# Optimization experiments

Measured on AMD Instinct MI355X. Metric: run time of the kernel, lower is better.

The kernel has to match this reference:

```python
import jax, jax.numpy as jnp
import numpy as np

B, T, D, U = 32, 2048, 512, 512


def setup_inputs() -> dict:
    key = jax.random.key(0)
    ks = jax.random.split(key, 6)
    value = jax.random.normal(ks[0], (B, T, D), dtype=jnp.float32)
    query = jax.random.normal(ks[1], (B, D), dtype=jnp.float32)
    mask = jax.random.randint(ks[2], (B, T), 0, 2, dtype=jnp.int32)
    # Glorot-ish scaled dense weights (no bias, matching Dense(use_bias=False))
    W1 = jax.random.normal(ks[3], (D, U), dtype=jnp.float32) * (1.0 / np.sqrt(D))
    W2 = jax.random.normal(ks[4], (D, U), dtype=jnp.float32) * (1.0 / np.sqrt(D))
    V = jax.random.normal(ks[5], (U,), dtype=jnp.float32) * (1.0 / np.sqrt(U))
    return {"value": value, "query": query, "mask": mask, "W1": W1, "W2": W2, "V": V}


def reference(value, query, mask, W1, W2, V):
    # Additive (Bahdanau) attention scores: u[b,t] = V . tanh(value[b,t] @ W1 + query[b] @ W2)
    w1_key = jnp.einsum('btd,du->btu', value, W1)          # [B, T, U]
    w2_query = jnp.einsum('bd,du->bu', query, W2)          # [B, U]
    u = jnp.einsum('btu,u->bt', jnp.tanh(w1_key + w2_query[:, None, :]), V)  # [B, T]
    # Masking: add -1e20 where mask == 0 (same as keras reference)
    u = u + (1.0 - mask.astype(u.dtype)) * jnp.asarray(-1e20, dtype=u.dtype)
    a = jax.nn.softmax(u, axis=1)                          # [B, T]
    # Pointer extraction: gather value row at argmax of attention weights
    idx = jnp.argmax(a, axis=1)                            # [B]
    context = jnp.take_along_axis(value, idx[:, None, None], axis=1)[:, 0, :]  # [B, D]
    return (context, a)
```

## Files before the change

kernel.cpp:

```cpp
#include <hip/hip_runtime.h>
#include <hip/hip_bf16.h>
#include <hip/hip_fp16.h>
#include <stdint.h>

#define B_ 32
#define T_ 2048
#define D_ 512
#define U_ 512
#define M_ (B_ * T_)

#define BM 64
#define BK 32
#define SAW 40
#define MAXC 4

typedef _Float16 half8  __attribute__((ext_vector_type(8)));
typedef _Float16 half4_t __attribute__((ext_vector_type(4)));
typedef float   floatx4 __attribute__((ext_vector_type(4)));

__device__ __forceinline__ float tanh_fast(float x) {
    float ax = fabsf(x);
    float e  = __expf(2.0f * ax);
    float t  = 1.0f - 2.0f / (e + 1.0f);
    return copysignf(t, x);
}

__device__ __forceinline__ void gld_lds16(const void* gsrc, void* lds_dst) {
    typedef __attribute__((address_space(1))) const char gch;
    typedef __attribute__((address_space(3))) char lch;
    __builtin_amdgcn_global_load_lds((const gch*)(uintptr_t)gsrc,
                                     (lch*)(uint32_t)(uintptr_t)lds_dst,
                                     16, 0, 0);
}

__global__ __launch_bounds__(256)
void k_prep(const float* __restrict__ W1, const float* __restrict__ query,
            const float* __restrict__ W2, _Float16* __restrict__ W1T,
            float* __restrict__ w2q) {
    const int bid = blockIdx.x;
    const int tid = threadIdx.x;
    if (bid < 64) {
        __shared__ float tile[64][65];
        const int bx = bid & 7;
        const int by = bid >> 3;
        const int k0 = bx * 64, n0 = by * 64;
        const int tx = tid & 63;
        const int ty = tid >> 6;
#pragma unroll
        for (int i = 0; i < 16; ++i) {
            int r = ty * 16 + i;
            tile[r][tx] = W1[(size_t)(k0 + r) * U_ + n0 + tx];
        }
        __syncthreads();
#pragma unroll
        for (int i = 0; i < 16; ++i) {
            int r = ty * 16 + i;
            W1T[(size_t)(n0 + r) * D_ + k0 + tx] = (_Float16)tile[tx][r];
        }
    } else {
        __shared__ float sq[D_];
        __shared__ float part[128];
        const int id = bid - 64;
        const int b  = id >> 2;
        const int nq = id & 3;
        sq[tid]       = query[b * D_ + tid];
        sq[tid + 256] = query[b * D_ + tid + 256];
        __syncthreads();
        const int n  = nq * 128 + (tid & 127);
        const int dh = tid >> 7;
        float acc = 0.f;
        const int d0 = dh * 256;
#pragma unroll 16
        for (int d = d0; d < d0 + 256; ++d)
            acc = fmaf(sq[d], W2[(size_t)d * U_ + n], acc);
        if (dh == 1) part[tid & 127] = acc;
        __syncthreads();
        if (dh == 0) w2q[b * U_ + n] = acc + part[tid];
    }
}

__global__ __launch_bounds__(512, 4)
void k_gemm_u(const float* __restrict__ value,
              const _Float16* __restrict__ W1T,
              const float* __restrict__ w2q,
              const float* __restrict__ Vv,
              float* __restrict__ u_out) {
    __shared__ __align__(16) _Float16 sA[2][BM * SAW];
    __shared__ __align__(16) _Float16 sB[2][U_ * BK];
    __shared__ float sRed[8][BM];

    const int tid  = threadIdx.x;
    const int wave = tid >> 6;
    const int lane = tid & 63;
    const int l15  = lane & 15;
    const int lg   = lane >> 4;
    const int m0   = blockIdx.x * BM;
    const int b    = m0 >> 11;

    const int bnl  = l15;
    const int bhi8 = lg * 8;

    const int ar = tid >> 3;
    const int ac = (tid & 7) * 4;
    const float* aptr = value + (size_t)(m0 + ar) * D_ + ac;

    floatx4 rA[2];

    rA[0] = *(const floatx4*)(aptr);
    rA[1] = *(const floatx4*)(aptr + BK);
#pragma unroll
    for (int jj = 0; jj < 4; ++jj) {
        const int inst = wave * 4 + jj;
        const int n = inst * 16 + bnl;
        gld_lds16(W1T + (size_t)n * D_ + bhi8, (void*)(&sB[0][inst * 512]));
    }
    {
        half4_t h;
        h[0] = (_Float16)rA[0][0]; h[1] = (_Float16)rA[0][1];
        h[2] = (_Float16)rA[0][2]; h[3] = (_Float16)rA[0][3];
        *(half4_t*)(&sA[0][ar * SAW + ac]) = h;
    }

    floatx4 acc[4][4];
    const floatx4 zero4 = {0.f, 0.f, 0.f, 0.f};
#pragma unroll
    for (int i = 0; i < 4; ++i)
#pragma unroll
        for (int j = 0; j < 4; ++j) acc[i][j] = zero4;

    __syncthreads();

    for (int kk = 0; kk < 16; ++kk) {
        const int cur = kk & 1;
        if (kk < 15) {
            const int k0n = (kk + 1) * BK;
#pragma unroll
            for (int jj = 0; jj < 4; ++jj) {
                const int inst = wave * 4 + jj;
                const int n = inst * 16 + bnl;
                gld_lds16(W1T + (size_t)n * D_ + k0n + bhi8,
                          (void*)(&sB[cur ^ 1][inst * 512]));
            }
        }
        if (kk < 14) rA[cur] = *(const floatx4*)(aptr + (kk + 2) * BK);

        half8 af[4], bf[4];
#pragma unroll
        for (int mi = 0; mi < 4; ++mi)
            af[mi] = *(const half8*)(&sA[cur][(mi * 16 + l15) * SAW + lg * 8]);
#pragma unroll
        for (int ni = 0; ni < 4; ++ni) {
            const int inst = wave * 4 + ni;
            bf[ni] = *(const half8*)(&sB[cur][inst * 512 + (lg * 16 + l15) * 8]);
        }
#pragma unroll
        for (int ni = 0; ni < 4; ++ni)
#pragma unroll
            for (int mi = 0; mi < 4; ++mi)
                acc[mi][ni] = __builtin_amdgcn_mfma_f32_16x16x32_f16(
                    af[mi], bf[ni], acc[mi][ni], 0, 0, 0);

        if (kk < 15) {
            const floatx4 v4 = rA[cur ^ 1];
            half4_t h;
            h[0] = (_Float16)v4[0]; h[1] = (_Float16)v4[1];
            h[2] = (_Float16)v4[2]; h[3] = (_Float16)v4[3];
            *(half4_t*)(&sA[cur ^ 1][ar * SAW + ac]) = h;
        }
        __syncthreads();
    }

    float ps[4][4];
#pragma unroll
    for (int mi = 0; mi < 4; ++mi)
#pragma unroll
        for (int j = 0; j < 4; ++j) ps[mi][j] = 0.f;

#pragma unroll
    for (int ni = 0; ni < 4; ++ni) {
        const int n = wave * 64 + ni * 16 + l15;
        const float w2 = w2q[b * U_ + n];
        const float vv = Vv[n];
#pragma unroll
        for (int mi = 0; mi < 4; ++mi)
#pragma unroll
            for (int j = 0; j < 4; ++j)
                ps[mi][j] += vv * tanh_fast(acc[mi][ni][j] + w2);
    }
#pragma unroll
    for (int off = 1; off < 16; off <<= 1)
#pragma unroll
        for (int mi = 0; mi < 4; ++mi)
#pragma unroll
            for (int j = 0; j < 4; ++j)
                ps[mi][j] += __shfl_xor(ps[mi][j], off, 64);

    if (l15 == 0) {
#pragma unroll
        for (int mi = 0; mi < 4; ++mi)
#pragma unroll
            for (int j = 0; j < 4; ++j)
                sRed[wave][mi * 16 + lg * 4 + j] = ps[mi][j];
    }
    __syncthreads();
    if (tid < BM) {
        float s = 0.f;
#pragma unroll
        for (int w = 0; w < 8; ++w) s += sRed[w][tid];
        u_out[m0 + tid] = s;
    }
}

__global__ __launch_bounds__(256)
void k_post(const float* __restrict__ u, const int* __restrict__ mask,
            const float* __restrict__ value, const float* __restrict__ W1,
            const float* __restrict__ w2q, const float* __restrict__ Vv,
            float* __restrict__ a_out, float* __restrict__ ctx_out) {
    __shared__ float sx[T_];
    __shared__ float rv[4];
    __shared__ int   ri[4];
    __shared__ float s_scalar;
    __shared__ int   s_cand[MAXC];
    __shared__ float s_score[MAXC];
    __shared__ __align__(16) float vrows[MAXC][D_];
    __shared__ int   s_t;

    const int b = blockIdx.x;
    const int tid = threadIdx.x;
    const int wave = tid >> 6, lane = tid & 63;

#pragma unroll
    for (int i = 0; i < 8; ++i) {
        const int t = tid * 8 + i;
        float x = u[b * T_ + t];
        if (mask[b * T_ + t] == 0) x = -1e20f;
        sx[t] = x;
    }
    __syncthreads();

    for (int r = 0; r < MAXC; ++r) {
        float v = -INFINITY; int vi = 0;
#pragma unroll
        for (int i = 0; i < 8; ++i) {
            const int t = tid * 8 + i;
            const float x = sx[t];
            if (x > v) { v = x; vi = t; }
        }
        for (int off = 32; off > 0; off >>= 1) {
            const float ov = __shfl_down(v, off, 64);
            const int   oi = __shfl_down(vi, off, 64);
            if (ov > v || (ov == v && oi < vi)) { v = ov; vi = oi; }
        }
        if (lane == 0) { rv[wave] = v; ri[wave] = vi; }
        __syncthreads();
        if (tid == 0) {
            float bv = rv[0]; int bi = ri[0];
            for (int w = 1; w < 4; ++w)
                if (rv[w] > bv || (rv[w] == bv && ri[w] < bi)) { bv = rv[w]; bi = ri[w]; }
            s_cand[r] = bi;
            if (r == 0) s_scalar = bv;
            sx[bi] = -INFINITY;
        }
        __syncthreads();
    }
    const float mx = s_scalar;

    float zloc = 0.f;
    float evals[8];
#pragma unroll
    for (int i = 0; i < 8; ++i) {
        const int t = tid * 8 + i;
        float x = u[b * T_ + t];
        if (mask[b * T_ + t] == 0) x = -1e20f;
        const float e = __expf(x - mx);
        evals[i] = e;
        zloc += e;
    }
    for (int off = 32; off > 0; off >>= 1) zloc += __shfl_down(zloc, off, 64);
    if (lane == 0) rv[wave] = zloc;
    __syncthreads();
    if (tid == 0) s_scalar = 1.0f / (rv[0] + rv[1] + rv[2] + rv[3]);
    __syncthreads();
    const float rz = s_scalar;
#pragma unroll
    for (int i = 0; i < 8; ++i) {
        const int t = tid * 8 + i;
        a_out[b * T_ + t] = evals[i] * rz;
    }

#pragma unroll
    for (int ci = 0; ci < MAXC; ++ci) {
        const int t = s_cand[ci];
        vrows[ci][tid]       = value[((size_t)b * T_ + t) * D_ + tid];
        vrows[ci][tid + 256] = value[((size_t)b * T_ + t) * D_ + tid + 256];
    }
    __syncthreads();

    float dots[2][MAXC];
#pragma unroll
    for (int j = 0; j < 2; ++j)
#pragma unroll
        for (int ci = 0; ci < MAXC; ++ci) dots[j][ci] = 0.f;

    for (int d4 = 0; d4 < D_; d4 += 4) {
        floatx4 vr[MAXC];
#pragma unroll
        for (int ci = 0; ci < MAXC; ++ci)
            vr[ci] = *(const floatx4*)(&vrows[ci][d4]);
#pragma unroll
        for (int k = 0; k < 4; ++k) {
            const float w0 = W1[(size_t)(d4 + k) * U_ + tid];
            const float w1 = W1[(size_t)(d4 + k) * U_ + tid + 256];
#pragma unroll
            for (int ci = 0; ci < MAXC; ++ci) {
                dots[0][ci] = fmaf(vr[ci][k], w0, dots[0][ci]);
                dots[1][ci] = fmaf(vr[ci][k], w1, dots[1][ci]);
            }
        }
    }
    float sc[MAXC];
#pragma unroll
    for (int ci = 0; ci < MAXC; ++ci) {
        const float n0v = Vv[tid]       * tanhf(dots[0][ci] + w2q[b * U_ + tid]);
        const float n1v = Vv[tid + 256] * tanhf(dots[1][ci] + w2q[b * U_ + tid + 256]);
        sc[ci] = n0v + n1v;
    }
#pragma unroll
    for (int ci = 0; ci < MAXC; ++ci)
        for (int off = 32; off > 0; off >>= 1)
            sc[ci] += __shfl_down(sc[ci], off, 64);
    __syncthreads();
    if (lane == 0) {
#pragma unroll
        for (int ci = 0; ci < MAXC; ++ci)
            vrows[ci][wave] = sc[ci];
    }
    __syncthreads();
    if (tid == 0) {
#pragma unroll
        for (int ci = 0; ci < MAXC; ++ci) {
            const int t = s_cand[ci];
            float s = vrows[ci][0] + vrows[ci][1] + vrows[ci][2] + vrows[ci][3];
            if (mask[b * T_ + t] == 0) s = -1e20f;
            s_score[ci] = s;
        }
        float bv = s_score[0]; int bt = s_cand[0];
        for (int i = 1; i < MAXC; ++i) {
            if (s_score[i] > bv || (s_score[i] == bv && s_cand[i] < bt)) {
                bv = s_score[i]; bt = s_cand[i];
            }
        }
        s_t = bt;
    }
    __syncthreads();

    const int t = s_t;
    ctx_out[b * D_ + tid]       = value[((size_t)b * T_ + t) * D_ + tid];
    ctx_out[b * D_ + tid + 256] = value[((size_t)b * T_ + t) * D_ + tid + 256];
}

extern "C" void kernel_launch(void* const* d_in, const int* in_sizes, int n_in,
                              void* d_out, int out_size, void* d_ws, size_t ws_size,
                              hipStream_t stream) {
    const float* value = (const float*)d_in[0];
    const float* query = (const float*)d_in[1];
    const int*   mask  = (const int*)d_in[2];
    const float* W1    = (const float*)d_in[3];
    const float* W2    = (const float*)d_in[4];
    const float* Vv    = (const float*)d_in[5];

    char* ws = (char*)d_ws;
    _Float16* W1T  = (_Float16*)ws;
    float*    w2q  = (float*)(ws + 524288);
    float*    u_ws = (float*)(ws + 524288 + 65536);

    float* ctx_out = (float*)d_out;
    float* a_out   = (float*)d_out + B_ * D_;

    hipLaunchKernelGGL(k_prep,   dim3(192), dim3(256), 0, stream,
                       W1, query, W2, W1T, w2q);
    hipLaunchKernelGGL(k_gemm_u, dim3(M_ / BM), dim3(512), 0, stream,
                       value, W1T, w2q, Vv, u_ws);
    hipLaunchKernelGGL(k_post,   dim3(32), dim3(256), 0, stream,
                       u_ws, mask, value, W1, w2q, Vv, a_out, ctx_out);
}
```

Before: 306.0 us.

## Rewrite GEMM as per-wave register-resident A tile with 32x32 MFMA, no LDS

Each wave now keeps its 32 rows of value, converted to fp16, fully in registers (32 half8 fragments). It streams W1T directly from global/L2 into 32x32x16 MFMAs for all 512 units and fuses tanh and the V dot product per 32-column group. LDS staging, double buffering and block-level syncs are gone, and the cross-wave reduction becomes a 32-lane shuffle reduce. In exchange, W1T is no longer shared through LDS, so every wave re-reads the full matrix from cache. The large register footprint also limits occupancy, and B-fragment loads are not prefetched or overlapped.

```diff
diff --git a/kernel.cpp b/kernel.cpp
--- a/kernel.cpp
+++ b/kernel.cpp
@@ -1,5 +1,4 @@
 #include <hip/hip_runtime.h>
-#include <hip/hip_bf16.h>
 #include <hip/hip_fp16.h>
 #include <stdint.h>
 
@@ -8,29 +7,17 @@
 #define D_ 512
 #define U_ 512
 #define M_ (B_ * T_)
-
-#define BM 64
-#define BK 32
-#define SAW 40
 #define MAXC 4
 
-typedef _Float16 half8  __attribute__((ext_vector_type(8)));
-typedef _Float16 half4_t __attribute__((ext_vector_type(4)));
-typedef float   floatx4 __attribute__((ext_vector_type(4)));
+typedef _Float16 half8   __attribute__((ext_vector_type(8)));
+typedef float   floatx4  __attribute__((ext_vector_type(4)));
+typedef float   floatx16 __attribute__((ext_vector_type(16)));
 
 __device__ __forceinline__ float tanh_fast(float x) {
     float ax = fabsf(x);
     float e  = __expf(2.0f * ax);
     float t  = 1.0f - 2.0f / (e + 1.0f);
     return copysignf(t, x);
-}
-
-__device__ __forceinline__ void gld_lds16(const void* gsrc, void* lds_dst) {
-    typedef __attribute__((address_space(1))) const char gch;
-    typedef __attribute__((address_space(3))) char lch;
-    __builtin_amdgcn_global_load_lds((const gch*)(uintptr_t)gsrc,
-                                     (lch*)(uint32_t)(uintptr_t)lds_dst,
-                                     16, 0, 0);
 }
 
 __global__ __launch_bounds__(256)
@@ -79,135 +66,81 @@
     }
 }
 
-__global__ __launch_bounds__(512, 4)
+__global__ __launch_bounds__(256, 2)
 void k_gemm_u(const float* __restrict__ value,
               const _Float16* __restrict__ W1T,
               const float* __restrict__ w2q,
               const float* __restrict__ Vv,
               float* __restrict__ u_out) {
-    __shared__ __align__(16) _Float16 sA[2][BM * SAW];
-    __shared__ __align__(16) _Float16 sB[2][U_ * BK];
-    __shared__ float sRed[8][BM];
-
     const int tid  = threadIdx.x;
     const int wave = tid >> 6;
     const int lane = tid & 63;
-    const int l15  = lane & 15;
-    const int lg   = lane >> 4;
-    const int m0   = blockIdx.x * BM;
+    const int l31  = lane & 31;
+    const int hi   = lane >> 5;
+    const int gw   = blockIdx.x * 4 + wave;
+    const int m0   = gw * 32;
     const int b    = m0 >> 11;
 
-    const int bnl  = l15;
-    const int bhi8 = lg * 8;
-
-    const int ar = tid >> 3;
-    const int ac = (tid & 7) * 4;
-    const float* aptr = value + (size_t)(m0 + ar) * D_ + ac;
-
-    floatx4 rA[2];
-
-    rA[0] = *(const floatx4*)(aptr);
-    rA[1] = *(const floatx4*)(aptr + BK);
-#pragma unroll
-    for (int jj = 0; jj < 4; ++jj) {
-        const int inst = wave * 4 + jj;
-        const int n = inst * 16 + bnl;
-        gld_lds16(W1T + (size_t)n * D_ + bhi8, (void*)(&sB[0][inst * 512]));
-    }
-    {
-        half4_t h;
-        h[0] = (_Float16)rA[0][0]; h[1] = (_Float16)rA[0][1];
-        h[2] = (_Float16)rA[0][2]; h[3] = (_Float16)rA[0][3];
-        *(half4_t*)(&sA[0][ar * SAW + ac]) = h;
-    }
-
-    floatx4 acc[4][4];
-    const floatx4 zero4 = {0.f, 0.f, 0.f, 0.f};
-#pragma unroll
-    for (int i = 0; i < 4; ++i)
-#pragma unroll
-        for (int j = 0; j < 4; ++j) acc[i][j] = zero4;
-
-    __syncthreads();
-
-    for (int kk = 0; kk < 16; ++kk) {
-        const int cur = kk & 1;
-        if (kk < 15) {
-            const int k0n = (kk + 1) * BK;
-#pragma unroll
-            for (int jj = 0; jj < 4; ++jj) {
-                const int inst = wave * 4 + jj;
-                const int n = inst * 16 + bnl;
-                gld_lds16(W1T + (size_t)n * D_ + k0n + bhi8,
-                          (void*)(&sB[cur ^ 1][inst * 512]));
+    half8 af[32];
+    const float* arow = value + (size_t)(m0 + l31) * D_ + hi * 8;
+#pragma unroll
+    for (int sb = 0; sb < 4; ++sb) {
+        floatx4 t0[8], t1[8];
+#pragma unroll
+        for (int s8 = 0; s8 < 8; ++s8) {
+            const float* p = arow + (sb * 8 + s8) * 16;
+            t0[s8] = *(const floatx4*)p;
+            t1[s8] = *(const floatx4*)(p + 4);
+        }
+#pragma unroll
+        for (int s8 = 0; s8 < 8; ++s8) {
+            half8 h;
+#pragma unroll
+            for (int j = 0; j < 4; ++j) {
+                h[j]     = (_Float16)t0[s8][j];
+                h[4 + j] = (_Float16)t1[s8][j];
             }
-        }
-        if (kk < 14) rA[cur] = *(const floatx4*)(aptr + (kk + 2) * BK);
-
-        half8 af[4], bf[4];
-#pragma unroll
-        for (int mi = 0; mi < 4; ++mi)
-            af[mi] = *(const half8*)(&sA[cur][(mi * 16 + l15) * SAW + lg * 8]);
-#pragma unroll
-        for (int ni = 0; ni < 4; ++ni) {
-            const int inst = wave * 4 + ni;
-            bf[ni] = *(const half8*)(&sB[cur][inst * 512 + (lg * 16 + l15) * 8]);
-        }
-#pragma unroll
-        for (int ni = 0; ni < 4; ++ni)
-#pragma unroll
-            for (int mi = 0; mi < 4; ++mi)
-                acc[mi][ni] = __builtin_amdgcn_mfma_f32_16x16x32_f16(
-                    af[mi], bf[ni], acc[mi][ni], 0, 0, 0);
-
-        if (kk < 15) {
-            const floatx4 v4 = rA[cur ^ 1];
-            half4_t h;
-            h[0] = (_Float16)v4[0]; h[1] = (_Float16)v4[1];
-            h[2] = (_Float16)v4[2]; h[3] = (_Float16)v4[3];
-            *(half4_t*)(&sA[cur ^ 1][ar * SAW + ac]) = h;
-        }
-        __syncthreads();
-    }
-
-    float ps[4][4];
-#pragma unroll
-    for (int mi = 0; mi < 4; ++mi)
-#pragma unroll
-        for (int j = 0; j < 4; ++j) ps[mi][j] = 0.f;
-
-#pragma unroll
-    for (int ni = 0; ni < 4; ++ni) {
-        const int n = wave * 64 + ni * 16 + l15;
+            af[sb * 8 + s8] = h;
+        }
+    }
+
+    float u_acc[16];
+#pragma unroll
+    for (int r = 0; r < 16; ++r) u_acc[r] = 0.f;
+
+    for (int g = 0; g < 16; ++g) {
+        const int n = g * 32 + l31;
+        const _Float16* bp = W1T + (size_t)n * D_ + hi * 8;
+
+        floatx16 acc;
+#pragma unroll
+        for (int r = 0; r < 16; ++r) acc[r] = 0.f;
+
+#pragma unroll
+        for (int s = 0; s < 32; ++s) {
+            const half8 bf = *(const half8*)(bp + s * 16);
+            acc = __builtin_amdgcn_mfma_f32_32x32x16_f16(af[s], bf, acc, 0, 0, 0);
+        }
+
         const float w2 = w2q[b * U_ + n];
         const float vv = Vv[n];
 #pragma unroll
-        for (int mi = 0; mi < 4; ++mi)
-#pragma unroll
-            for (int j = 0; j < 4; ++j)
-                ps[mi][j] += vv * tanh_fast(acc[mi][ni][j] + w2);
-    }
-#pragma unroll
-    for (int off = 1; off < 16; off <<= 1)
-#pragma unroll
-        for (int mi = 0; mi < 4; ++mi)
-#pragma unroll
-            for (int j = 0; j < 4; ++j)
-                ps[mi][j] += __shfl_xor(ps[mi][j], off, 64);
-
-    if (l15 == 0) {
-#pragma unroll
-        for (int mi = 0; mi < 4; ++mi)
-#pragma unroll
-            for (int j = 0; j < 4; ++j)
-                sRed[wave][mi * 16 + lg * 4 + j] = ps[mi][j];
-    }
-    __syncthreads();
-    if (tid < BM) {
-        float s = 0.f;
-#pragma unroll
-        for (int w = 0; w < 8; ++w) s += sRed[w][tid];
-        u_out[m0 + tid] = s;
+        for (int r = 0; r < 16; ++r)
+            u_acc[r] += vv * tanh_fast(acc[r] + w2);
+    }
+
+#pragma unroll
+    for (int off = 1; off < 32; off <<= 1)
+#pragma unroll
+        for (int r = 0; r < 16; ++r)
+            u_acc[r] += __shfl_xor(u_acc[r], off, 64);
+
+    if (l31 == 0) {
+#pragma unroll
+        for (int r = 0; r < 16; ++r) {
+            const int row = (r & 3) + 8 * (r >> 2) + 4 * hi;
+            u_out[m0 + row] = u_acc[r];
+        }
     }
 }
 
@@ -379,7 +312,7 @@
 
     hipLaunchKernelGGL(k_prep,   dim3(192), dim3(256), 0, stream,
                        W1, query, W2, W1T, w2q);
-    hipLaunchKernelGGL(k_gemm_u, dim3(M_ / BM), dim3(512), 0, stream,
+    hipLaunchKernelGGL(k_gemm_u, dim3(512), dim3(256), 0, stream,
                        value, W1T, w2q, Vv, u_ws);
     hipLaunchKernelGGL(k_post,   dim3(32), dim3(256), 0, stream,
                        u_ws, mask, value, W1, w2q, Vv, a_out, ctx_out);
```

Result: slower. 361.6 us (+18.2%).

## Split GEMM N dimension across two blocks, drop double buffering, sum partial scores

Applied to the files above, without the earlier changes.

The fused GEMM+tanh+V-dot kernel now gives each 64-row tile to two blocks, each covering half of the U columns (256). The two blocks write separate partial score vectors, and the post kernel adds them. LDS double buffering and register prefetch are removed to cut LDS and register use so more blocks fit per CU (launch bounds 4→5), and the grid doubles to 2048 blocks. The cost is that each 64-row value tile is read and converted twice, and load latency is no longer overlapped within a block.

```diff
diff --git a/kernel.cpp b/kernel.cpp
--- a/kernel.cpp
+++ b/kernel.cpp
@@ -1,5 +1,4 @@
 #include <hip/hip_runtime.h>
-#include <hip/hip_bf16.h>
 #include <hip/hip_fp16.h>
 #include <stdint.h>
 
@@ -8,15 +7,14 @@
 #define D_ 512
 #define U_ 512
 #define M_ (B_ * T_)
-
-#define BM 64
+#define MAXC 4
+
 #define BK 32
 #define SAW 40
-#define MAXC 4
-
-typedef _Float16 half8  __attribute__((ext_vector_type(8)));
+
+typedef _Float16 half8   __attribute__((ext_vector_type(8)));
 typedef _Float16 half4_t __attribute__((ext_vector_type(4)));
-typedef float   floatx4 __attribute__((ext_vector_type(4)));
+typedef float   floatx4  __attribute__((ext_vector_type(4)));
 
 __device__ __forceinline__ float tanh_fast(float x) {
     float ax = fabsf(x);
@@ -79,22 +77,25 @@
     }
 }
 
-__global__ __launch_bounds__(512, 4)
+__global__ __launch_bounds__(512, 5)
 void k_gemm_u(const float* __restrict__ value,
               const _Float16* __restrict__ W1T,
               const float* __restrict__ w2q,
               const float* __restrict__ Vv,
-              float* __restrict__ u_out) {
-    __shared__ __align__(16) _Float16 sA[2][BM * SAW];
-    __shared__ __align__(16) _Float16 sB[2][U_ * BK];
-    __shared__ float sRed[8][BM];
+              float* __restrict__ u_part) {
+    __shared__ __align__(16) _Float16 sA[64 * SAW];
+    __shared__ __align__(16) _Float16 sB[256 * BK];
+    __shared__ float sRed[8][64];
 
     const int tid  = threadIdx.x;
     const int wave = tid >> 6;
     const int lane = tid & 63;
     const int l15  = lane & 15;
     const int lg   = lane >> 4;
-    const int m0   = blockIdx.x * BM;
+    const int bx   = blockIdx.x;
+    const int sl   = (bx >> 3) & 1;
+    const int rg   = ((bx >> 4) << 3) | (bx & 7);
+    const int m0   = rg * 64;
     const int b    = m0 >> 11;
 
     const int bnl  = l15;
@@ -104,70 +105,46 @@
     const int ac = (tid & 7) * 4;
     const float* aptr = value + (size_t)(m0 + ar) * D_ + ac;
 
-    floatx4 rA[2];
-
-    rA[0] = *(const floatx4*)(aptr);
-    rA[1] = *(const floatx4*)(aptr + BK);
-#pragma unroll
-    for (int jj = 0; jj < 4; ++jj) {
-        const int inst = wave * 4 + jj;
-        const int n = inst * 16 + bnl;
-        gld_lds16(W1T + (size_t)n * D_ + bhi8, (void*)(&sB[0][inst * 512]));
-    }
-    {
-        half4_t h;
-        h[0] = (_Float16)rA[0][0]; h[1] = (_Float16)rA[0][1];
-        h[2] = (_Float16)rA[0][2]; h[3] = (_Float16)rA[0][3];
-        *(half4_t*)(&sA[0][ar * SAW + ac]) = h;
-    }
-
-    floatx4 acc[4][4];
+    floatx4 acc[4][2];
     const floatx4 zero4 = {0.f, 0.f, 0.f, 0.f};
 #pragma unroll
     for (int i = 0; i < 4; ++i)
 #pragma unroll
-        for (int j = 0; j < 4; ++j) acc[i][j] = zero4;
-
-    __syncthreads();
-
-    for (int kk = 0; kk < 16; ++kk) {
-        const int cur = kk & 1;
-        if (kk < 15) {
-            const int k0n = (kk + 1) * BK;
-#pragma unroll
-            for (int jj = 0; jj < 4; ++jj) {
-                const int inst = wave * 4 + jj;
-                const int n = inst * 16 + bnl;
-                gld_lds16(W1T + (size_t)n * D_ + k0n + bhi8,
-                          (void*)(&sB[cur ^ 1][inst * 512]));
-            }
-        }
-        if (kk < 14) rA[cur] = *(const floatx4*)(aptr + (kk + 2) * BK);
-
-        half8 af[4], bf[4];
+        for (int j = 0; j < 2; ++j) acc[i][j] = zero4;
+
+    for (int it = 0; it < 16; ++it) {
+        const int k0 = it * BK;
+        __syncthreads();
+        {
+            const floatx4 v4 = *(const floatx4*)(aptr + k0);
+            half4_t h;
+            h[0] = (_Float16)v4[0]; h[1] = (_Float16)v4[1];
+            h[2] = (_Float16)v4[2]; h[3] = (_Float16)v4[3];
+            *(half4_t*)(&sA[ar * SAW + ac]) = h;
+        }
+#pragma unroll
+        for (int jj = 0; jj < 2; ++jj) {
+            const int inst = wave * 2 + jj;
+            const int n = sl * 256 + inst * 16 + bnl;
+            gld_lds16(W1T + (size_t)n * D_ + k0 + bhi8, (void*)(&sB[inst * 512]));
+        }
+        __syncthreads();
+
+        half8 af[4], bf[2];
 #pragma unroll
         for (int mi = 0; mi < 4; ++mi)
-            af[mi] = *(const half8*)(&sA[cur][(mi * 16 + l15) * SAW + lg * 8]);
-#pragma unroll
-        for (int ni = 0; ni < 4; ++ni) {
-            const int inst = wave * 4 + ni;
-            bf[ni] = *(const half8*)(&sB[cur][inst * 512 + (lg * 16 + l15) * 8]);
-        }
-#pragma unroll
-        for (int ni = 0; ni < 4; ++ni)
+            af[mi] = *(const half8*)(&sA[(mi * 16 + l15) * SAW + lg * 8]);
+#pragma unroll
+        for (int ni = 0; ni < 2; ++ni) {
+            const int inst = wave * 2 + ni;
+            bf[ni] = *(const half8*)(&sB[inst * 512 + (lg * 16 + l15) * 8]);
+        }
+#pragma unroll
+        for (int ni = 0; ni < 2; ++ni)
 #pragma unroll
             for (int mi = 0; mi < 4; ++mi)
                 acc[mi][ni] = __builtin_amdgcn_mfma_f32_16x16x32_f16(
                     af[mi], bf[ni], acc[mi][ni], 0, 0, 0);
-
-        if (kk < 15) {
-            const floatx4 v4 = rA[cur ^ 1];
-            half4_t h;
-            h[0] = (_Float16)v4[0]; h[1] = (_Float16)v4[1];
-            h[2] = (_Float16)v4[2]; h[3] = (_Float16)v4[3];
-            *(half4_t*)(&sA[cur ^ 1][ar * SAW + ac]) = h;
-        }
-        __syncthreads();
     }
 
     float ps[4][4];
@@ -177,8 +154,8 @@
         for (int j = 0; j < 4; ++j) ps[mi][j] = 0.f;
 
 #pragma unroll
-    for (int ni = 0; ni < 4; ++ni) {
-        const int n = wave * 64 + ni * 16 + l15;
+    for (int ni = 0; ni < 2; ++ni) {
+        const int n = sl * 256 + wave * 32 + ni * 16 + l15;
         const float w2 = w2q[b * U_ + n];
         const float vv = Vv[n];
 #pragma unroll
@@ -203,16 +180,16 @@
                 sRed[wave][mi * 16 + lg * 4 + j] = ps[mi][j];
     }
     __syncthreads();
-    if (tid < BM) {
+    if (tid < 64) {
         float s = 0.f;
 #pragma unroll
         for (int w = 0; w < 8; ++w) s += sRed[w][tid];
-        u_out[m0 + tid] = s;
+        u_part[(size_t)sl * M_ + m0 + tid] = s;
     }
 }
 
 __global__ __launch_bounds__(256)
-void k_post(const float* __restrict__ u, const int* __restrict__ mask,
+void k_post(const float* __restrict__ u_part, const int* __restrict__ mask,
             const float* __restrict__ value, const float* __restrict__ W1,
             const float* __restrict__ w2q, const float* __restrict__ Vv,
             float* __restrict__ a_out, float* __restrict__ ctx_out) {
@@ -232,7 +209,7 @@
 #pragma unroll
     for (int i = 0; i < 8; ++i) {
         const int t = tid * 8 + i;
-        float x = u[b * T_ + t];
+        float x = u_part[b * T_ + t] + u_part[M_ + b * T_ + t];
         if (mask[b * T_ + t] == 0) x = -1e20f;
         sx[t] = x;
     }
@@ -270,7 +247,7 @@
 #pragma unroll
     for (int i = 0; i < 8; ++i) {
         const int t = tid * 8 + i;
-        float x = u[b * T_ + t];
+        float x = u_part[b * T_ + t] + u_part[M_ + b * T_ + t];
         if (mask[b * T_ + t] == 0) x = -1e20f;
         const float e = __expf(x - mx);
         evals[i] = e;
@@ -370,17 +347,17 @@
     const float* Vv    = (const float*)d_in[5];
 
     char* ws = (char*)d_ws;
-    _Float16* W1T  = (_Float16*)ws;
-    float*    w2q  = (float*)(ws + 524288);
-    float*    u_ws = (float*)(ws + 524288 + 65536);
+    _Float16* W1T    = (_Float16*)ws;
+    float*    w2q    = (float*)(ws + 524288);
+    float*    u_part = (float*)(ws + 524288 + 65536);
 
     float* ctx_out = (float*)d_out;
     float* a_out   = (float*)d_out + B_ * D_;
 
     hipLaunchKernelGGL(k_prep,   dim3(192), dim3(256), 0, stream,
                        W1, query, W2, W1T, w2q);
-    hipLaunchKernelGGL(k_gemm_u, dim3(M_ / BM), dim3(512), 0, stream,
-                       value, W1T, w2q, Vv, u_ws);
+    hipLaunchKernelGGL(k_gemm_u, dim3(2048), dim3(512), 0, stream,
+                       value, W1T, w2q, Vv, u_part);
     hipLaunchKernelGGL(k_post,   dim3(32), dim3(256), 0, stream,
-                       u_ws, mask, value, W1, w2q, Vv, a_out, ctx_out);
-}
+                       u_part, mask, value, W1, w2q, Vv, a_out, ctx_out);
+}
```

Measured after the change: 331.7 us. 1.08x slower.
